# Optimization experiments

Hardware: AMD Instinct MI355X
Metric: run time of the kernel (lower is better)

The kernel has to match this reference:

```python
import jax, jax.numpy as jnp
import numpy as np

D_MODEL = 768
N_HEADS = 12
D_HEAD = 64
INIT_RANGE = 0.02
IGNORE = -100000.0


def setup_inputs() -> dict:
    key = jax.random.key(0)
    ks = jax.random.split(key, 5)
    x = jax.random.normal(ks[0], (2, 2048, D_MODEL), dtype=jnp.float32)
    W_Q = INIT_RANGE * jax.random.normal(ks[1], (N_HEADS, D_MODEL, D_HEAD), dtype=jnp.float32)
    W_K = INIT_RANGE * jax.random.normal(ks[2], (N_HEADS, D_MODEL, D_HEAD), dtype=jnp.float32)
    W_V = INIT_RANGE * jax.random.normal(ks[3], (N_HEADS, D_MODEL, D_HEAD), dtype=jnp.float32)
    W_O = INIT_RANGE * jax.random.normal(ks[4], (N_HEADS, D_HEAD, D_MODEL), dtype=jnp.float32)
    b_Q = jnp.zeros((N_HEADS, D_HEAD), dtype=jnp.float32)
    b_K = jnp.zeros((N_HEADS, D_HEAD), dtype=jnp.float32)
    b_V = jnp.zeros((N_HEADS, D_HEAD), dtype=jnp.float32)
    b_O = jnp.zeros((D_MODEL,), dtype=jnp.float32)
    return {"x": x, "W_Q": W_Q, "b_Q": b_Q, "W_K": W_K, "b_K": b_K,
            "W_V": W_V, "b_V": b_V, "W_O": W_O, "b_O": b_O}


def reference(x, W_Q, b_Q, W_K, b_K, W_V, b_V, W_O, b_O):
    # x: [b, s, m]; W_*: [h, m, d]
    Q = jnp.einsum('bsm,hmd->bshd', x, W_Q) + b_Q  # [b, s, h, d]
    K = jnp.einsum('bsm,hmd->bshd', x, W_K) + b_K
    V = jnp.einsum('bsm,hmd->bshd', x, W_V) + b_V
    scores = jnp.einsum('bqhd,bkhd->bhqk', Q, K) / jnp.sqrt(jnp.float32(D_HEAD))
    s = scores.shape[-1]
    causal = jnp.triu(jnp.ones((s, s), dtype=bool), k=1)  # True above diagonal
    scores = jnp.where(causal, jnp.float32(IGNORE), scores)
    pattern = jax.nn.softmax(scores, axis=-1)  # [b, h, q, k]
    Z = jnp.einsum('bhqk,bkhd->bqhd', pattern, V)
    out = jnp.einsum('bqhd,hdm->bqm', Z, W_O) + b_O
    return out
```

## Files before the change

kernel.cpp:

```cpp
#include <hip/hip_runtime.h>
#include <hip/hip_bf16.h>

#define BATCH 2
#define SLEN 2048
#define NH 12
#define DM 768
#define DH 64
#define ROWS (BATCH*SLEN)
#define NQKV (3*DM)
#define NCHUNK 80

typedef __attribute__((ext_vector_type(8))) short bf16x8;
typedef __attribute__((ext_vector_type(4))) float f32x4;
typedef unsigned short u16;
typedef unsigned int u32;
typedef __attribute__((ext_vector_type(4))) unsigned short u16x4;
typedef __attribute__((ext_vector_type(8))) unsigned short u16x8;

__device__ __forceinline__ u16 f2b(float f) {
    unsigned int u = __builtin_bit_cast(unsigned int, f);
    unsigned int r = (u + 0x7FFFu + ((u >> 16) & 1u)) >> 16;
    return (u16)r;
}
__device__ __forceinline__ float b2f(u16 v) {
    unsigned int u = ((unsigned int)v) << 16;
    return __builtin_bit_cast(float, u);
}

__device__ __forceinline__ void gload16(const u16* g, u16* l) {
    __builtin_amdgcn_global_load_lds(
        (const __attribute__((address_space(1))) unsigned int*)g,
        (__attribute__((address_space(3))) unsigned int*)l,
        16, 0, 0);
}


__global__ __launch_bounds__(256) void pack_x(const float* __restrict__ x, u16* __restrict__ xb) {
    int i = blockIdx.x * 256 + threadIdx.x;
    const float4* xv = (const float4*)x;
    float4 a = xv[i * 2], b = xv[i * 2 + 1];
    u16x8 o;
    o[0] = f2b(a.x); o[1] = f2b(a.y); o[2] = f2b(a.z); o[3] = f2b(a.w);
    o[4] = f2b(b.x); o[5] = f2b(b.y); o[6] = f2b(b.z); o[7] = f2b(b.w);
    *(u16x8*)(xb + (size_t)i * 8) = o;
}

__global__ __launch_bounds__(256) void pack_wqkv(const float* __restrict__ WQ, const float* __restrict__ WK,
                                                 const float* __restrict__ WV, u16* __restrict__ out) {
    __shared__ u16 L[64 * 72];
    int mt = blockIdx.x, h = blockIdx.y, sel = blockIdx.z;
    const float* W = sel == 0 ? WQ : (sel == 1 ? WK : WV);
    const float* src = W + ((size_t)h * DM + mt * 64) * DH;
    int t = threadIdx.x;
    for (int j = 0; j < 4; j++) {
        int i = t + 256 * j;
        int r = i >> 4, cf = i & 15;
        float4 v = ((const float4*)src)[i];
        u16x4 o; o[0] = f2b(v.x); o[1] = f2b(v.y); o[2] = f2b(v.z); o[3] = f2b(v.w);
        *(u16x4*)&L[r * 72 + cf * 4] = o;
    }
    __syncthreads();
    u16* orow = out + ((size_t)(sel * DM + h * DH)) * DM + mt * 64;
    for (int j = 0; j < 16; j++) {
        int e = t + 256 * j;
        int d = e >> 6, mm = e & 63;
        orow[(size_t)d * DM + mm] = L[mm * 72 + d];
    }
}

__global__ __launch_bounds__(256) void pack_wo(const float* __restrict__ WO, u16* __restrict__ out) {
    __shared__ u16 L[64 * 72];
    int bi = blockIdx.x, bj = blockIdx.y;
    int t = threadIdx.x;
    for (int j = 0; j < 4; j++) {
        int i = t + 256 * j;
        int r = i >> 4, cf = i & 15;
        float4 v = ((const float4*)(WO + (size_t)(bi * 64 + r) * DM + bj * 64))[cf];
        u16x4 o; o[0] = f2b(v.x); o[1] = f2b(v.y); o[2] = f2b(v.z); o[3] = f2b(v.w);
        *(u16x4*)&L[r * 72 + cf * 4] = o;
    }
    __syncthreads();
    for (int j = 0; j < 16; j++) {
        int e = t + 256 * j;
        int c = e >> 6, r = e & 63;
        out[(size_t)(bj * 64 + c) * DM + bi * 64 + r] = L[r * 72 + c];
    }
}


__global__ __launch_bounds__(256) void gemm_qkv(const u16* __restrict__ A, const u16* __restrict__ Bt,
                                                const float* __restrict__ bQ, const float* __restrict__ bK,
                                                const float* __restrict__ bV,
                                                u16* __restrict__ Qb, u16* __restrict__ Kb, u16* __restrict__ Vb) {
    __shared__ u16 Al[128 * 64];
    __shared__ u16 Bl[128 * 64];
    int t = threadIdx.x;
    int n0 = blockIdx.x * 128, m0 = blockIdx.y * 128;
    int lane = t & 63, w = t >> 6;
    int ln = lane & 15, qd = lane >> 4;
    int wr = (w & 1) * 64, wc = (w >> 1) * 64;
    int srow = lane >> 3, slot = lane & 7;
    f32x4 acc[4][4] = {};

    for (int kt = 0; kt < DM / 64; kt++) {
        __syncthreads();
        for (int j = 0; j < 4; j++) {
            int r = w * 32 + j * 8 + srow;
            int gc = slot ^ (r & 7);
            gload16(A + (size_t)(m0 + r) * DM + kt * 64 + gc * 8, &Al[(w * 32 + j * 8) * 64]);
            gload16(Bt + (size_t)(n0 + r) * DM + kt * 64 + gc * 8, &Bl[(w * 32 + j * 8) * 64]);
        }
        __syncthreads();
        for (int ks = 0; ks < 2; ks++) {
            int sl = ((ks * 4 + qd) ^ (ln & 7)) * 8;
            bf16x8 af[4], bfr[4];
            for (int rt = 0; rt < 4; rt++)
                af[rt] = *(const bf16x8*)&Al[(wr + rt * 16 + ln) * 64 + sl];
            for (int ct = 0; ct < 4; ct++)
                bfr[ct] = *(const bf16x8*)&Bl[(wc + ct * 16 + ln) * 64 + sl];
            for (int rt = 0; rt < 4; rt++)
                for (int ct = 0; ct < 4; ct++)
                    acc[rt][ct] = __builtin_amdgcn_mfma_f32_16x16x32_bf16(af[rt], bfr[ct], acc[rt][ct], 0, 0, 0);
        }
    }
    int sel = n0 / DM;
    if (sel == 2) {
        for (int ct = 0; ct < 4; ct++) {
            int col = n0 - 2 * DM + wc + ct * 16 + ln;
            int hh = col >> 6, dd = col & 63;
            float bv = bV[col];
            for (int rt = 0; rt < 4; rt++) {
                int row = m0 + wr + rt * 16 + qd * 4;
                int bb = row >> 11, ss = row & 2047;
                u16x4 pk;
                for (int r = 0; r < 4; r++) pk[r] = f2b(acc[rt][ct][r] + bv);
                *(u16x4*)&Vb[(((size_t)bb * NH + hh) * DH + dd) * SLEN + ss] = pk;
            }
        }
    } else {
        const float* bias = sel == 0 ? bQ : bK;
        u16* Out = sel == 0 ? Qb : Kb;
        const float qs = sel == 0 ? 0.125f * 1.44269504f : 1.0f;
        for (int ct = 0; ct < 4; ct++) {
            int col = n0 - sel * DM + wc + ct * 16 + ln;
            int hh = col >> 6, dd = col & 63;
            float bv = bias[col];
            for (int rt = 0; rt < 4; rt++) {
                int row = m0 + wr + rt * 16 + qd * 4;
                for (int r = 0; r < 4; r++) {
                    int rg = row + r;
                    int bb = rg >> 11, ss = rg & 2047;
                    Out[(((size_t)bb * NH + hh) * SLEN + ss) * DH + dd] = f2b((acc[rt][ct][r] + bv) * qs);
                }
            }
        }
    }
}


__device__ __forceinline__ void cid2qc(int cid, int& qt, int& c, int& nc) {
    if (cid < 8)       { qt = cid;                 c = 0;              nc = 1; }
    else if (cid < 24) { qt = 8 + ((cid - 8) >> 1); c = (cid - 8) & 1; nc = 2; }
    else if (cid < 48) { qt = 16 + (cid - 24) / 3;  c = (cid - 24) % 3; nc = 3; }
    else               { qt = 24 + ((cid - 48) >> 2); c = (cid - 48) & 3; nc = 4; }
}

__global__ __launch_bounds__(256, 4) void attn(const u16* __restrict__ Qb, const u16* __restrict__ Kb,
                                               const u16* __restrict__ Vtg,
                                               u16* __restrict__ Po, float* __restrict__ Plv) {
    __shared__ u16 Kl[64 * 72];
    __shared__ u16 Vt[64 * 72];
    __shared__ u16 Pq[4][16 * 72];
    int cid = blockIdx.x, bh = blockIdx.y;
    int qt, c, nc;
    cid2qc(cid, qt, c, nc);
    int ntiles = qt + 1;
    int kt0 = c * ntiles / nc, kt1 = (c + 1) * ntiles / nc;
    const u16* Qp = Qb + (size_t)bh * SLEN * DH;
    const u16* Kp = Kb + (size_t)bh * SLEN * DH;
    const u16* Vp = Vtg + (size_t)bh * SLEN * DH;
    int t = threadIdx.x, lane = t & 63, w = t >> 6;
    int ln = lane & 15, qd = lane >> 4;
    int qw = qt * 64 + w * 16;

    bf16x8 qf[2];
    for (int ks = 0; ks < 2; ks++)
        qf[ks] = *(const bf16x8*)(Qp + (size_t)(qw + ln) * DH + ks * 32 + qd * 8);

    float l = 0.f;
    f32x4 o[4] = {};

    u16x8 kr[2], vr[2];
    int sr = t >> 3, scf = t & 7;
    auto preload = [&](int kt) {
        int k0 = kt * 64;
        for (int j = 0; j < 2; j++) {
            int r = sr + 32 * j;
            kr[j] = *(const u16x8*)(Kp + (size_t)(k0 + r) * DH + scf * 8);
            vr[j] = *(const u16x8*)(Vp + (size_t)r * SLEN + k0 + scf * 8);
        }
    };
    preload(kt0);

    u16* Pw = Pq[w];
    for (int kt = kt0; kt < kt1; kt++) {
        __syncthreads();
        for (int j = 0; j < 2; j++) {
            int r = sr + 32 * j;
            *(u16x8*)&Kl[r * 72 + scf * 8] = kr[j];
            *(u16x8*)&Vt[r * 72 + scf * 8] = vr[j];
        }
        __syncthreads();
        if (kt + 1 < kt1) preload(kt + 1);

        f32x4 sf[4] = {};
        for (int ks = 0; ks < 2; ks++)
            for (int ct = 0; ct < 4; ct++) {
                bf16x8 kf = *(const bf16x8*)&Kl[(ct * 16 + ln) * 72 + ks * 32 + qd * 8];
                sf[ct] = __builtin_amdgcn_mfma_f32_16x16x32_bf16(kf, qf[ks], sf[ct], 0, 0, 0);
            }

        if (kt == qt) {
            int qg = qw + ln;
            for (int ct = 0; ct < 4; ct++)
                for (int r = 0; r < 4; r++) {
                    int kg = kt * 64 + ct * 16 + qd * 4 + r;
                    if (kg > qg) sf[ct][r] = -1e30f;
                }
        }

        float s = 0.f;
        for (int ct = 0; ct < 4; ct++) {
            u32 eb[4];
            for (int r = 0; r < 4; r++) {
                float e = exp2f(sf[ct][r]);
                u32 ub = __builtin_bit_cast(u32, e) & 0xFFFF0000u;
                eb[r] = __builtin_bit_cast(u32, e);
                s += __builtin_bit_cast(float, ub);
            }
            u32 p01 = __builtin_amdgcn_perm(eb[1], eb[0], 0x07060302u);
            u32 p23 = __builtin_amdgcn_perm(eb[3], eb[2], 0x07060302u);
            uint2 pk; pk.x = p01; pk.y = p23;
            *(uint2*)&Pw[ln * 72 + ct * 16 + qd * 4] = pk;
        }
        l += s;

        for (int ks = 0; ks < 2; ks++) {
            bf16x8 pf = *(const bf16x8*)&Pw[ln * 72 + ks * 32 + qd * 8];
            for (int dt = 0; dt < 4; dt++) {
                bf16x8 vf = *(const bf16x8*)&Vt[(dt * 16 + ln) * 72 + ks * 32 + qd * 8];
                o[dt] = __builtin_amdgcn_mfma_f32_16x16x32_bf16(vf, pf, o[dt], 0, 0, 0);
            }
        }
    }

    l += __shfl_xor(l, 16, 64);
    l += __shfl_xor(l, 32, 64);

    size_t pid = (size_t)bh * NCHUNK + cid;
    u16* op = Po + pid * 4096;
    for (int dt = 0; dt < 4; dt++) {
        u16x4 ov;
        ov[0] = f2b(o[dt][0]); ov[1] = f2b(o[dt][1]);
        ov[2] = f2b(o[dt][2]); ov[3] = f2b(o[dt][3]);
        *(u16x4*)&op[(w * 16 + ln) * 64 + dt * 16 + qd * 4] = ov;
    }
    if (qd == 0)
        Plv[pid * 64 + w * 16 + ln] = l;
}


__global__ __launch_bounds__(256) void combine(const u16* __restrict__ Po, const float* __restrict__ Plv,
                                               u16* __restrict__ Zb) {
    int qt = blockIdx.x, bh = blockIdx.y;
    int b = bh / NH, h = bh % NH;
    int nc = (qt >> 3) + 1;
    int base;
    if (qt < 8) base = qt;
    else if (qt < 16) base = 8 + (qt - 8) * 2;
    else if (qt < 24) base = 24 + (qt - 16) * 3;
    else base = 48 + (qt - 24) * 4;
    int t = threadIdx.x;
    int q = t >> 2, dseg = (t & 3) * 16;

    float acc[16] = {};
    float lsum = 0.f;
    for (int cc = 0; cc < nc; cc++) {
        size_t pid = (size_t)bh * NCHUNK + base + cc;
        lsum += Plv[pid * 64 + q];
        const u16* op = Po + pid * 4096 + q * 64 + dseg;
        for (int j = 0; j < 2; j++) {
            u16x8 v = *(const u16x8*)(op + j * 8);
            for (int e = 0; e < 8; e++)
                acc[j * 8 + e] += b2f(v[e]);
        }
    }
    float inv = 1.0f / lsum;
    u16* Zp = Zb + ((size_t)b * SLEN + qt * 64 + q) * DM + h * DH + dseg;
    u16x8 ov;
    for (int j = 0; j < 2; j++) {
        for (int e = 0; e < 8; e++) ov[e] = f2b(acc[j * 8 + e] * inv);
        *(u16x8*)(Zp + j * 8) = ov;
    }
}


__global__ __launch_bounds__(256) void gemm_proj(const u16* __restrict__ A, const u16* __restrict__ Bt,
                                                 const float* __restrict__ bO, float* __restrict__ out) {
    __shared__ u16 Al[64 * 64];
    __shared__ u16 Bl[96 * 64];
    int t = threadIdx.x;
    int n0 = blockIdx.x * 96, m0 = blockIdx.y * 64;
    int lane = t & 63, w = t >> 6;
    int ln = lane & 15, qd = lane >> 4;
    int wr = (w & 1) * 32, wc = (w >> 1) * 48;
    int srow = lane >> 3, slot = lane & 7;
    f32x4 acc[2][3] = {};

    for (int kt = 0; kt < DM / 64; kt++) {
        __syncthreads();
        for (int j = 0; j < 2; j++) {
            int r = w * 16 + j * 8 + srow;
            int gc = slot ^ (r & 7);
            gload16(A + (size_t)(m0 + r) * DM + kt * 64 + gc * 8, &Al[(w * 16 + j * 8) * 64]);
        }
        for (int j = 0; j < 3; j++) {
            int r = w * 24 + j * 8 + srow;
            int gc = slot ^ (r & 7);
            gload16(Bt + (size_t)(n0 + r) * DM + kt * 64 + gc * 8, &Bl[(w * 24 + j * 8) * 64]);
        }
        __syncthreads();
        for (int ks = 0; ks < 2; ks++) {
            int sl = ((ks * 4 + qd) ^ (ln & 7)) * 8;
            bf16x8 af[2], bfr[3];
            for (int rt = 0; rt < 2; rt++)
                af[rt] = *(const bf16x8*)&Al[(wr + rt * 16 + ln) * 64 + sl];
            for (int ct = 0; ct < 3; ct++)
                bfr[ct] = *(const bf16x8*)&Bl[(wc + ct * 16 + ln) * 64 + sl];
            for (int rt = 0; rt < 2; rt++)
                for (int ct = 0; ct < 3; ct++)
                    acc[rt][ct] = __builtin_amdgcn_mfma_f32_16x16x32_bf16(af[rt], bfr[ct], acc[rt][ct], 0, 0, 0);
        }
    }
    for (int ct = 0; ct < 3; ct++) {
        int col = n0 + wc + ct * 16 + ln;
        float bv = bO[col];
        for (int rt = 0; rt < 2; rt++) {
            int row = m0 + wr + rt * 16 + qd * 4;
            for (int r = 0; r < 4; r++)
                out[(size_t)(row + r) * DM + col] = acc[rt][ct][r] + bv;
        }
    }
}


extern "C" void kernel_launch(void* const* d_in, const int* in_sizes, int n_in,
                              void* d_out, int out_size, void* d_ws, size_t ws_size,
                              hipStream_t stream) {
    const float* x  = (const float*)d_in[0];
    const float* WQ = (const float*)d_in[1];
    const float* bQ = (const float*)d_in[2];
    const float* WK = (const float*)d_in[3];
    const float* bK = (const float*)d_in[4];
    const float* WV = (const float*)d_in[5];
    const float* bV = (const float*)d_in[6];
    const float* WO = (const float*)d_in[7];
    const float* bO = (const float*)d_in[8];
    float* out = (float*)d_out;

    u16* xb   = (u16*)d_ws;
    u16* wqkv = xb + (size_t)ROWS * DM;
    u16* wo   = wqkv + (size_t)NQKV * DM;
    u16* Qb   = wo + (size_t)DM * DM;
    size_t hsz = (size_t)BATCH * NH * SLEN * DH;
    u16* Kb   = Qb + hsz;
    u16* Vb   = Kb + hsz;
    u16* Zb   = Vb + hsz;
    u16* Po   = Zb + (size_t)ROWS * DM;
    float* Pl = (float*)(Po + (size_t)BATCH * NH * NCHUNK * 4096);

    pack_x<<<ROWS * DM / 2048, 256, 0, stream>>>(x, xb);
    pack_wqkv<<<dim3(12, 12, 3), 256, 0, stream>>>(WQ, WK, WV, wqkv);
    pack_wo<<<dim3(12, 12), 256, 0, stream>>>(WO, wo);
    gemm_qkv<<<dim3(NQKV / 128, ROWS / 128), 256, 0, stream>>>(xb, wqkv, bQ, bK, bV, Qb, Kb, Vb);
    attn<<<dim3(NCHUNK, BATCH * NH), 256, 0, stream>>>(Qb, Kb, Vb, Po, Pl);
    combine<<<dim3(SLEN / 64, BATCH * NH), 256, 0, stream>>>(Po, Pl, Zb);
    gemm_proj<<<dim3(DM / 96, ROWS / 64), 256, 0, stream>>>(Zb, wo, bO, out);
}
```

Before: 173.5 us.

## Process 128 query rows per attention block with swizzled direct-to-LDS K/V loads

The attention kernel now gives each wave two 16-row query tiles, so a block covers 128 queries, each K/V tile is reused twice, and the number of chunks halves. K/V are loaded with gload16 (likely a direct global-to-LDS load) into an XOR-swizzled unpadded layout instead of register prefetch with padding. The combine kernel and partial buffers are resized to match. This cuts K/V traffic and per-block overhead, but drops the register double-buffering, lowers block count and parallelism, and raises register pressure.

After: 180.7 us. 1.04x slower.

```diff
diff --git a/kernel.cpp b/kernel.cpp
--- a/kernel.cpp
+++ b/kernel.cpp
@@ -8,7 +8,7 @@
 #define DH 64
 #define ROWS (BATCH*SLEN)
 #define NQKV (3*DM)
-#define NCHUNK 80
+#define NCHUNK 40
 
 typedef __attribute__((ext_vector_type(8))) short bf16x8;
 typedef __attribute__((ext_vector_type(4))) float f32x4;
@@ -158,147 +158,163 @@
 }
 
 
-__device__ __forceinline__ void cid2qc(int cid, int& qt, int& c, int& nc) {
-    if (cid < 8)       { qt = cid;                 c = 0;              nc = 1; }
-    else if (cid < 24) { qt = 8 + ((cid - 8) >> 1); c = (cid - 8) & 1; nc = 2; }
-    else if (cid < 48) { qt = 16 + (cid - 24) / 3;  c = (cid - 24) % 3; nc = 3; }
-    else               { qt = 24 + ((cid - 48) >> 2); c = (cid - 48) & 3; nc = 4; }
+__device__ __forceinline__ void cid2qc(int cid, int& p, int& c, int& nc) {
+    if (cid < 4)       { p = cid;                  c = 0;               nc = 1; }
+    else if (cid < 12) { p = 4 + ((cid - 4) >> 1);  c = (cid - 4) & 1;   nc = 2; }
+    else if (cid < 24) { p = 8 + (cid - 12) / 3;    c = (cid - 12) % 3;  nc = 3; }
+    else               { p = 12 + ((cid - 24) >> 2); c = (cid - 24) & 3; nc = 4; }
 }
 
 __global__ __launch_bounds__(256, 4) void attn(const u16* __restrict__ Qb, const u16* __restrict__ Kb,
                                                const u16* __restrict__ Vtg,
                                                u16* __restrict__ Po, float* __restrict__ Plv) {
-    __shared__ u16 Kl[64 * 72];
-    __shared__ u16 Vt[64 * 72];
-    __shared__ u16 Pq[4][16 * 72];
+    __shared__ u16 Kl[64 * 64];
+    __shared__ u16 Vt[64 * 64];
+    __shared__ u16 Pq[4 * 32 * 72];
     int cid = blockIdx.x, bh = blockIdx.y;
-    int qt, c, nc;
-    cid2qc(cid, qt, c, nc);
-    int ntiles = qt + 1;
+    int p, c, nc;
+    cid2qc(cid, p, c, nc);
+    int ntiles = 2 * p + 2;
     int kt0 = c * ntiles / nc, kt1 = (c + 1) * ntiles / nc;
     const u16* Qp = Qb + (size_t)bh * SLEN * DH;
     const u16* Kp = Kb + (size_t)bh * SLEN * DH;
     const u16* Vp = Vtg + (size_t)bh * SLEN * DH;
     int t = threadIdx.x, lane = t & 63, w = t >> 6;
     int ln = lane & 15, qd = lane >> 4;
-    int qw = qt * 64 + w * 16;
-
-    bf16x8 qf[2];
-    for (int ks = 0; ks < 2; ks++)
-        qf[ks] = *(const bf16x8*)(Qp + (size_t)(qw + ln) * DH + ks * 32 + qd * 8);
-
-    float l = 0.f;
-    f32x4 o[4] = {};
-
-    u16x8 kr[2], vr[2];
-    int sr = t >> 3, scf = t & 7;
-    auto preload = [&](int kt) {
+    int srow = lane >> 3, slot = lane & 7;
+    int qbA = p * 128 + w * 32, qbB = qbA + 16;
+
+    bf16x8 qfA[2], qfB[2];
+    for (int ks = 0; ks < 2; ks++) {
+        qfA[ks] = *(const bf16x8*)(Qp + (size_t)(qbA + ln) * DH + ks * 32 + qd * 8);
+        qfB[ks] = *(const bf16x8*)(Qp + (size_t)(qbB + ln) * DH + ks * 32 + qd * 8);
+    }
+
+    float lA = 0.f, lB = 0.f;
+    f32x4 oA[4] = {}, oB[4] = {};
+
+    u16* PwA = Pq + w * 32 * 72;
+    u16* PwB = PwA + 16 * 72;
+
+    for (int kt = kt0; kt < kt1; kt++) {
         int k0 = kt * 64;
+        __syncthreads();
         for (int j = 0; j < 2; j++) {
-            int r = sr + 32 * j;
-            kr[j] = *(const u16x8*)(Kp + (size_t)(k0 + r) * DH + scf * 8);
-            vr[j] = *(const u16x8*)(Vp + (size_t)r * SLEN + k0 + scf * 8);
-        }
-    };
-    preload(kt0);
-
-    u16* Pw = Pq[w];
-    for (int kt = kt0; kt < kt1; kt++) {
-        __syncthreads();
-        for (int j = 0; j < 2; j++) {
-            int r = sr + 32 * j;
-            *(u16x8*)&Kl[r * 72 + scf * 8] = kr[j];
-            *(u16x8*)&Vt[r * 72 + scf * 8] = vr[j];
-        }
-        __syncthreads();
-        if (kt + 1 < kt1) preload(kt + 1);
-
-        f32x4 sf[4] = {};
-        for (int ks = 0; ks < 2; ks++)
+            int r = w * 16 + j * 8 + srow;
+            int gc = slot ^ (r & 7);
+            gload16(Kp + (size_t)(k0 + r) * DH + gc * 8, &Kl[(w * 16 + j * 8) * 64]);
+            gload16(Vp + (size_t)r * SLEN + k0 + gc * 8, &Vt[(w * 16 + j * 8) * 64]);
+        }
+        __syncthreads();
+
+        f32x4 sfA[4] = {}, sfB[4] = {};
+        for (int ks = 0; ks < 2; ks++) {
+            int sl = ((ks * 4 + qd) ^ (ln & 7)) * 8;
             for (int ct = 0; ct < 4; ct++) {
-                bf16x8 kf = *(const bf16x8*)&Kl[(ct * 16 + ln) * 72 + ks * 32 + qd * 8];
-                sf[ct] = __builtin_amdgcn_mfma_f32_16x16x32_bf16(kf, qf[ks], sf[ct], 0, 0, 0);
+                bf16x8 kf = *(const bf16x8*)&Kl[(ct * 16 + ln) * 64 + sl];
+                sfA[ct] = __builtin_amdgcn_mfma_f32_16x16x32_bf16(kf, qfA[ks], sfA[ct], 0, 0, 0);
+                sfB[ct] = __builtin_amdgcn_mfma_f32_16x16x32_bf16(kf, qfB[ks], sfB[ct], 0, 0, 0);
             }
-
-        if (kt == qt) {
-            int qg = qw + ln;
+        }
+
+        if (kt >= (qbA >> 6)) {
+            int qg = qbA + ln;
             for (int ct = 0; ct < 4; ct++)
                 for (int r = 0; r < 4; r++) {
-                    int kg = kt * 64 + ct * 16 + qd * 4 + r;
-                    if (kg > qg) sf[ct][r] = -1e30f;
+                    int kg = k0 + ct * 16 + qd * 4 + r;
+                    if (kg > qg) sfA[ct][r] = -1e30f;
                 }
         }
-
-        float s = 0.f;
+        if (kt >= (qbB >> 6)) {
+            int qg = qbB + ln;
+            for (int ct = 0; ct < 4; ct++)
+                for (int r = 0; r < 4; r++) {
+                    int kg = k0 + ct * 16 + qd * 4 + r;
+                    if (kg > qg) sfB[ct][r] = -1e30f;
+                }
+        }
+
+        float sA = 0.f, sB = 0.f;
         for (int ct = 0; ct < 4; ct++) {
-            u32 eb[4];
+            u32 ea[4], eb[4];
             for (int r = 0; r < 4; r++) {
-                float e = exp2f(sf[ct][r]);
-                u32 ub = __builtin_bit_cast(u32, e) & 0xFFFF0000u;
-                eb[r] = __builtin_bit_cast(u32, e);
-                s += __builtin_bit_cast(float, ub);
+                float eA = exp2f(sfA[ct][r]);
+                float eB = exp2f(sfB[ct][r]);
+                ea[r] = __builtin_bit_cast(u32, eA);
+                eb[r] = __builtin_bit_cast(u32, eB);
+                sA += __builtin_bit_cast(float, ea[r] & 0xFFFF0000u);
+                sB += __builtin_bit_cast(float, eb[r] & 0xFFFF0000u);
             }
-            u32 p01 = __builtin_amdgcn_perm(eb[1], eb[0], 0x07060302u);
-            u32 p23 = __builtin_amdgcn_perm(eb[3], eb[2], 0x07060302u);
-            uint2 pk; pk.x = p01; pk.y = p23;
-            *(uint2*)&Pw[ln * 72 + ct * 16 + qd * 4] = pk;
-        }
-        l += s;
+            uint2 pkA, pkB;
+            pkA.x = __builtin_amdgcn_perm(ea[1], ea[0], 0x07060302u);
+            pkA.y = __builtin_amdgcn_perm(ea[3], ea[2], 0x07060302u);
+            pkB.x = __builtin_amdgcn_perm(eb[1], eb[0], 0x07060302u);
+            pkB.y = __builtin_amdgcn_perm(eb[3], eb[2], 0x07060302u);
+            *(uint2*)&PwA[ln * 72 + ct * 16 + qd * 4] = pkA;
+            *(uint2*)&PwB[ln * 72 + ct * 16 + qd * 4] = pkB;
+        }
+        lA += sA; lB += sB;
 
         for (int ks = 0; ks < 2; ks++) {
-            bf16x8 pf = *(const bf16x8*)&Pw[ln * 72 + ks * 32 + qd * 8];
+            int sl = ((ks * 4 + qd) ^ (ln & 7)) * 8;
+            bf16x8 pfA = *(const bf16x8*)&PwA[ln * 72 + ks * 32 + qd * 8];
+            bf16x8 pfB = *(const bf16x8*)&PwB[ln * 72 + ks * 32 + qd * 8];
             for (int dt = 0; dt < 4; dt++) {
-                bf16x8 vf = *(const bf16x8*)&Vt[(dt * 16 + ln) * 72 + ks * 32 + qd * 8];
-                o[dt] = __builtin_amdgcn_mfma_f32_16x16x32_bf16(vf, pf, o[dt], 0, 0, 0);
+                bf16x8 vf = *(const bf16x8*)&Vt[(dt * 16 + ln) * 64 + sl];
+                oA[dt] = __builtin_amdgcn_mfma_f32_16x16x32_bf16(vf, pfA, oA[dt], 0, 0, 0);
+                oB[dt] = __builtin_amdgcn_mfma_f32_16x16x32_bf16(vf, pfB, oB[dt], 0, 0, 0);
             }
         }
     }
 
-    l += __shfl_xor(l, 16, 64);
-    l += __shfl_xor(l, 32, 64);
+    lA += __shfl_xor(lA, 16, 64);
+    lA += __shfl_xor(lA, 32, 64);
+    lB += __shfl_xor(lB, 16, 64);
+    lB += __shfl_xor(lB, 32, 64);
 
     size_t pid = (size_t)bh * NCHUNK + cid;
-    u16* op = Po + pid * 4096;
+    u16* op = Po + pid * 8192;
     for (int dt = 0; dt < 4; dt++) {
-        u16x4 ov;
-        ov[0] = f2b(o[dt][0]); ov[1] = f2b(o[dt][1]);
-        ov[2] = f2b(o[dt][2]); ov[3] = f2b(o[dt][3]);
-        *(u16x4*)&op[(w * 16 + ln) * 64 + dt * 16 + qd * 4] = ov;
-    }
-    if (qd == 0)
-        Plv[pid * 64 + w * 16 + ln] = l;
+        u16x4 ovA, ovB;
+        for (int r = 0; r < 4; r++) { ovA[r] = f2b(oA[dt][r]); ovB[r] = f2b(oB[dt][r]); }
+        *(u16x4*)&op[(w * 32 + ln) * 64 + dt * 16 + qd * 4] = ovA;
+        *(u16x4*)&op[(w * 32 + 16 + ln) * 64 + dt * 16 + qd * 4] = ovB;
+    }
+    if (qd == 0) {
+        Plv[pid * 128 + w * 32 + ln] = lA;
+        Plv[pid * 128 + w * 32 + 16 + ln] = lB;
+    }
 }
 
 
 __global__ __launch_bounds__(256) void combine(const u16* __restrict__ Po, const float* __restrict__ Plv,
                                                u16* __restrict__ Zb) {
-    int qt = blockIdx.x, bh = blockIdx.y;
+    int p = blockIdx.x, bh = blockIdx.y;
     int b = bh / NH, h = bh % NH;
-    int nc = (qt >> 3) + 1;
-    int base;
-    if (qt < 8) base = qt;
-    else if (qt < 16) base = 8 + (qt - 8) * 2;
-    else if (qt < 24) base = 24 + (qt - 16) * 3;
-    else base = 48 + (qt - 24) * 4;
+    int nc, base;
+    if (p < 4)       { base = p;                  nc = 1; }
+    else if (p < 8)  { base = 4 + (p - 4) * 2;    nc = 2; }
+    else if (p < 12) { base = 12 + (p - 8) * 3;   nc = 3; }
+    else             { base = 24 + (p - 12) * 4;  nc = 4; }
     int t = threadIdx.x;
-    int q = t >> 2, dseg = (t & 3) * 16;
-
-    float acc[16] = {};
+    int q = t >> 1, dseg = (t & 1) * 32;
+
+    float acc[32] = {};
     float lsum = 0.f;
     for (int cc = 0; cc < nc; cc++) {
         size_t pid = (size_t)bh * NCHUNK + base + cc;
-        lsum += Plv[pid * 64 + q];
-        const u16* op = Po + pid * 4096 + q * 64 + dseg;
-        for (int j = 0; j < 2; j++) {
+        lsum += Plv[pid * 128 + q];
+        const u16* op = Po + pid * 8192 + q * 64 + dseg;
+        for (int j = 0; j < 4; j++) {
             u16x8 v = *(const u16x8*)(op + j * 8);
             for (int e = 0; e < 8; e++)
                 acc[j * 8 + e] += b2f(v[e]);
         }
     }
     float inv = 1.0f / lsum;
-    u16* Zp = Zb + ((size_t)b * SLEN + qt * 64 + q) * DM + h * DH + dseg;
-    u16x8 ov;
-    for (int j = 0; j < 2; j++) {
+    u16* Zp = Zb + ((size_t)b * SLEN + p * 128 + q) * DM + h * DH + dseg;
+    for (int j = 0; j < 4; j++) {
+        u16x8 ov;
         for (int e = 0; e < 8; e++) ov[e] = f2b(acc[j * 8 + e] * inv);
         *(u16x8*)(Zp + j * 8) = ov;
     }
@@ -377,13 +393,13 @@
     u16* Vb   = Kb + hsz;
     u16* Zb   = Vb + hsz;
     u16* Po   = Zb + (size_t)ROWS * DM;
-    float* Pl = (float*)(Po + (size_t)BATCH * NH * NCHUNK * 4096);
+    float* Pl = (float*)(Po + (size_t)BATCH * NH * NCHUNK * 8192);
 
     pack_x<<<ROWS * DM / 2048, 256, 0, stream>>>(x, xb);
     pack_wqkv<<<dim3(12, 12, 3), 256, 0, stream>>>(WQ, WK, WV, wqkv);
     pack_wo<<<dim3(12, 12), 256, 0, stream>>>(WO, wo);
     gemm_qkv<<<dim3(NQKV / 128, ROWS / 128), 256, 0, stream>>>(xb, wqkv, bQ, bK, bV, Qb, Kb, Vb);
     attn<<<dim3(NCHUNK, BATCH * NH), 256, 0, stream>>>(Qb, Kb, Vb, Po, Pl);
-    combine<<<dim3(SLEN / 64, BATCH * NH), 256, 0, stream>>>(Po, Pl, Zb);
+    combine<<<dim3(SLEN / 128, BATCH * NH), 256, 0, stream>>>(Po, Pl, Zb);
     gemm_proj<<<dim3(DM / 96, ROWS / 64), 256, 0, stream>>>(Zb, wo, bO, out);
 }
```
